# Optimization experiments

Hardware: AMD Instinct MI355X
Metric: run time of the kernel (lower is better)

Reference implementation:

```python
import jax, jax.numpy as jnp
import numpy as np

N = 100000   # nodes
E = 1600000  # edges
F = 64       # input_features == output_features
BN_EPS = 1e-5


def _bn(x, gamma, beta):
    # torch BatchNorm1d (training mode): biased batch statistics
    mu = jnp.mean(x, axis=0)
    var = jnp.var(x, axis=0)
    return (x - mu) * jax.lax.rsqrt(var + BN_EPS) * gamma + beta


def setup_inputs() -> dict:
    key = jax.random.key(0)
    ks = jax.random.split(key, 16)
    s = 0.05
    inp = {
        'node_feats': jax.random.normal(ks[0], (N, F), jnp.float32),
        'edge_feats': jax.random.normal(ks[1], (E, F), jnp.float32),
        'src': jax.random.randint(ks[2], (E,), 0, N, jnp.int32),
        'dst': jax.random.randint(ks[3], (E,), 0, N, jnp.int32),
        # linear params: W [F_in, F_out], b [F_out]
        'W_src_gate': jax.random.normal(ks[4], (F, F), jnp.float32) * s,
        'b_src_gate': jnp.zeros((F,), jnp.float32),
        'W_dst_gate': jax.random.normal(ks[5], (F, F), jnp.float32) * s,
        'b_dst_gate': jnp.zeros((F,), jnp.float32),
        'W_edge_gate': jax.random.normal(ks[6], (F, F), jnp.float32) * s,
        'b_edge_gate': jnp.zeros((F,), jnp.float32),
        'W_src_update': jax.random.normal(ks[7], (F, F), jnp.float32) * s,
        'b_src_update': jnp.zeros((F,), jnp.float32),
        'W_dst_update': jax.random.normal(ks[8], (F, F), jnp.float32) * s,
        'b_dst_update': jnp.zeros((F,), jnp.float32),
        'bn_nodes_gamma': jnp.ones((F,), jnp.float32),
        'bn_nodes_beta': jnp.zeros((F,), jnp.float32),
        'bn_edges_gamma': jnp.ones((F,), jnp.float32),
        'bn_edges_beta': jnp.zeros((F,), jnp.float32),
    }
    return inp


def reference(node_feats, edge_feats, src, dst,
              W_src_gate, b_src_gate, W_dst_gate, b_dst_gate,
              W_edge_gate, b_edge_gate, W_src_update, b_src_update,
              W_dst_update, b_dst_update,
              bn_nodes_gamma, bn_nodes_beta, bn_edges_gamma, bn_edges_beta):
    # EdgeGatedGraphConv (arXiv:1711.07553), residual=True
    e_src = node_feats @ W_src_gate + b_src_gate          # [N,F]
    e_dst = node_feats @ W_dst_gate + b_dst_gate          # [N,F]
    # u_add_v gather + edge transform -> gate logits m [E,F]
    m = e_src[src] + e_dst[dst] + (edge_feats @ W_edge_gate + b_edge_gate)
    sigma = jax.nn.sigmoid(m)                             # [E,F]
    Bh = node_feats @ W_dst_update + b_dst_update         # [N,F]
    # u_mul_e message + scatter-sum to destination nodes
    sum_sigma_h = jax.ops.segment_sum(Bh[src] * sigma, dst, num_segments=node_feats.shape[0])
    sum_sigma = jax.ops.segment_sum(sigma, dst, num_segments=node_feats.shape[0])
    h = sum_sigma_h / (sum_sigma + 1e-6)                  # normalized aggregation
    x = node_feats @ W_src_update + b_src_update + h
    x = jax.nn.silu(_bn(x, bn_nodes_gamma, bn_nodes_beta))
    y = jax.nn.silu(_bn(m, bn_edges_gamma, bn_edges_beta))
    x = node_feats + x   # residual
    y = edge_feats + y   # residual
    return (x, y)
```

## Files before the change

kernel.cpp:

```cpp
#include <hip/hip_runtime.h>
#include <hip/hip_bf16.h>

typedef __attribute__((ext_vector_type(8))) __bf16 bf16x8;
typedef __attribute__((ext_vector_type(4))) float f32x4;

#define MFMA(a,b,c) __builtin_amdgcn_mfma_f32_16x16x32_bf16((a),(b),(c),0,0,0)

__device__ __forceinline__ bf16x8 cvt8(float4 a, float4 b){
  bf16x8 r;
  r[0]=(__bf16)a.x; r[1]=(__bf16)a.y; r[2]=(__bf16)a.z; r[3]=(__bf16)a.w;
  r[4]=(__bf16)b.x; r[5]=(__bf16)b.y; r[6]=(__bf16)b.z; r[7]=(__bf16)b.w;
  return r;
}

__global__ void setup_k(const float* __restrict__ W_sg, const float* __restrict__ W_dg,
                        const float* __restrict__ W_eg, const float* __restrict__ W_su,
                        const float* __restrict__ W_du,
                        bf16x8* __restrict__ Wq,
                        int4* __restrict__ zp, int nz4){
  if (blockIdx.x < 16){
    int tid = blockIdx.x*256 + threadIdx.x;
    if (tid >= 2560) return;
    int lane = tid & 63, g = lane>>4, c = lane&15;
    int frag = (tid>>6)&7, m = tid>>9;
    const float* Ws[5] = {W_eg, W_sg, W_dg, W_du, W_su};
    const float* W = Ws[m];
    int mt = frag>>1, kh = frag&1;
    bf16x8 v;
    #pragma unroll
    for (int j=0;j<8;j++) v[j] = (__bf16)W[(kh*32+g*8+j)*64 + mt*16 + c];
    Wq[tid] = v;
  } else {
    int i = (blockIdx.x-16)*256 + threadIdx.x, st = (gridDim.x-16)*256;
    for (; i<nz4; i+=st) zp[i] = make_int4(0,0,0,0);
  }
}

__global__ __launch_bounds__(256) void xform_hist_k(
    const float* __restrict__ nf, const bf16x8* __restrict__ Wq,
    __bf16* __restrict__ es16, __bf16* __restrict__ ed16,
    __bf16* __restrict__ bh16, float* __restrict__ A_src, int ntiles, int nxf,
    const int* __restrict__ dst, int* __restrict__ cnt, int E)
{
  if ((int)blockIdx.x < nxf){
    int lane = threadIdx.x & 63;
    int gw = blockIdx.x*4 + (threadIdx.x>>6);
    if (gw >= ntiles) return;
    int g = lane>>4, c = lane&15;
    long base = (long)gw*16;
    const float* rp = nf + (base + c)*64 + g*8;
    float4 a0 = *(const float4*)rp,      a1 = *(const float4*)(rp+4);
    float4 a2 = *(const float4*)(rp+32), a3 = *(const float4*)(rp+36);
    bf16x8 B0 = cvt8(a0,a1), B1 = cvt8(a2,a3);
    __bf16* outs[3] = {es16, ed16, bh16};
    const int mats[3] = {1,2,3};
    #pragma unroll
    for (int i=0;i<3;i++){
      #pragma unroll
      for (int mt=0;mt<4;mt++){
        f32x4 am = {0.f,0.f,0.f,0.f};
        am = MFMA(Wq[(mats[i]*8+mt*2+0)*64+lane], B0, am);
        am = MFMA(Wq[(mats[i]*8+mt*2+1)*64+lane], B1, am);
        union { __bf16 h[4]; uint2 u; } pk;
        #pragma unroll
        for (int e=0;e<4;e++) pk.h[e] = (__bf16)am[e];
        *(uint2*)(outs[i] + (base+c)*64 + mt*16 + 4*g) = pk.u;
      }
    }
    #pragma unroll
    for (int mt=0;mt<4;mt++){
      f32x4 am = {0.f,0.f,0.f,0.f};
      am = MFMA(Wq[(4*8+mt*2+0)*64+lane], B0, am);
      am = MFMA(Wq[(4*8+mt*2+1)*64+lane], B1, am);
      *(float4*)(A_src + (base+c)*64 + mt*16 + 4*g) =
        make_float4(am[0],am[1],am[2],am[3]);
    }
  } else {
    int nb = gridDim.x - nxf;
    int i = (blockIdx.x-nxf)*256 + threadIdx.x, st = nb*256;
    for (; i<E; i+=st) atomicAdd(&cnt[dst[i]], 1);
  }
}

__global__ __launch_bounds__(1024) void scan_k(const int* __restrict__ cnt,
                                               int* __restrict__ row, int Nn){
  __shared__ int part[1024];
  int t = threadIdx.x;
  int C = (Nn + 1023) >> 10;
  int lo = t*C;
  int hi = lo + C; if (hi > Nn) hi = Nn;
  int s = 0;
  for (int i=lo; i<hi; i++) s += cnt[i];
  part[t] = s;
  __syncthreads();
  for (int off=1; off<1024; off<<=1){
    int v = part[t];
    int u = (t>=off) ? part[t-off] : 0;
    __syncthreads();
    part[t] = v + u;
    __syncthreads();
  }
  int excl = (t==0) ? 0 : part[t-1];
  for (int i=lo; i<hi; i++){ row[i] = excl; excl += cnt[i]; }
  if (t==1023) row[Nn] = excl;
}

struct T2 {
  float4 e0,e1,e2,e3;
  bf16x8 bs0,bs1,bd0,bd1;
};

__device__ __forceinline__ T2 ld_t2(const float* __restrict__ ef,
                                    const __bf16* __restrict__ es16,
                                    const __bf16* __restrict__ ed16,
                                    long base, int c, int g, int sc, int dc){
  T2 t;
  const float* rpe = ef + (base+c)*64 + g*8;
  t.e0=*(const float4*)rpe;      t.e1=*(const float4*)(rpe+4);
  t.e2=*(const float4*)(rpe+32); t.e3=*(const float4*)(rpe+36);
  t.bs0 = *(const bf16x8*)(es16 + (long)sc*64 + g*8);
  t.bs1 = *(const bf16x8*)(es16 + (long)sc*64 + 32 + g*8);
  t.bd0 = *(const bf16x8*)(ed16 + (long)dc*64 + g*8);
  t.bd1 = *(const bf16x8*)(ed16 + (long)dc*64 + 32 + g*8);
  return t;
}

#define NFILL 1024
__global__ __launch_bounds__(256) void fillA_k(
    const int* __restrict__ src, const int* __restrict__ dst,
    const int* __restrict__ rowp, int* __restrict__ cnt2,
    int2* __restrict__ pairs, int E,
    const float* __restrict__ ef,
    const __bf16* __restrict__ es16, const __bf16* __restrict__ ed16,
    const float* __restrict__ b_sg, const float* __restrict__ b_dg,
    const float* __restrict__ b_eg,
    const bf16x8* __restrict__ Wq,
    __bf16* __restrict__ m16, int ntiles)
{
  __shared__ bf16x8 wl[8*64];
  __shared__ uint2 mst[4][256];
  if (blockIdx.x < NFILL){
    int i = blockIdx.x*256 + threadIdx.x, st = NFILL*256;
    for (; i<E; i+=st){
      int d = dst[i];
      int pos = rowp[d] + atomicAdd(&cnt2[d], 1);
      pairs[pos] = make_int2(i, src[i]);
    }
    return;
  }
  {
    int t = threadIdx.x;
    #pragma unroll
    for (int i=0;i<2;i++) wl[i*256+t] = Wq[i*256+t];
  }
  __syncthreads();
  int lane = threadIdx.x & 63, g = lane>>4, c = lane&15;
  int wv = threadIdx.x>>6;
  bf16x8 I0, I1;
  #pragma unroll
  for (int j=0;j<8;j++){
    I0[j] = (g*8+j == c)      ? (__bf16)1.0f : (__bf16)0.0f;
    I1[j] = (g*8+j == 16 + c) ? (__bf16)1.0f : (__bf16)0.0f;
  }
  int gw = (blockIdx.x-NFILL)*4 + wv;
  int nw = (gridDim.x-NFILL)*4;
  float bias2[4][4];
  #pragma unroll
  for (int mt=0;mt<4;mt++)
    #pragma unroll
    for (int e=0;e<4;e++){
      int f = mt*16 + 4*g + e;
      bias2[mt][e] = b_sg[f] + b_dg[f] + b_eg[f];
    }
  if (gw >= ntiles) return;
  int sc = src[(long)gw*16 + c], dc = dst[(long)gw*16 + c];
  T2 cur = ld_t2(ef, es16, ed16, (long)gw*16, c, g, sc, dc);
  int t1i = gw + nw;
  int sn = sc, dn = dc;
  if (t1i < ntiles){ sn = src[(long)t1i*16 + c]; dn = dst[(long)t1i*16 + c]; }
  int r_o = lane>>3;
  int u0_o = (lane&7)*2;
  for (int tt=gw; tt<ntiles; tt+=nw){
    int t1 = tt + nw;
    T2 nxt;
    if (t1 < ntiles) nxt = ld_t2(ef, es16, ed16, (long)t1*16, c, g, sn, dn);
    int t2 = t1 + nw;
    if (t2 < ntiles){ sn = src[(long)t2*16 + c]; dn = dst[(long)t2*16 + c]; }
    bf16x8 BE0=cvt8(cur.e0,cur.e1), BE1=cvt8(cur.e2,cur.e3);
    #pragma unroll
    for (int mt=0;mt<4;mt++){
      bf16x8 Is = (mt&1) ? I1 : I0;
      f32x4 am = {0.f,0.f,0.f,0.f};
      am = MFMA(wl[(mt*2+0)*64+lane], BE0, am);
      am = MFMA(wl[(mt*2+1)*64+lane], BE1, am);
      am = MFMA(Is, (mt>>1) ? cur.bs1 : cur.bs0, am);
      am = MFMA(Is, (mt>>1) ? cur.bd1 : cur.bd0, am);
      union { __bf16 h[4]; uint2 u; } pk;
      #pragma unroll
      for (int e=0;e<4;e++) pk.h[e] = (__bf16)(am[e] + bias2[mt][e]);
      int u = mt*4 + g;
      mst[wv][c*16 + (u^c)] = pk.u;
    }
    char* tb = (char*)m16 + (size_t)tt*16*128;
    #pragma unroll
    for (int k=0;k<2;k++){
      int r = k*8 + r_o;
      uint2 a = mst[wv][r*16 + ( u0_o      ^ r)];
      uint2 b = mst[wv][r*16 + ((u0_o + 1) ^ r)];
      *(uint4*)(tb + k*1024 + lane*16) = make_uint4(a.x,a.y,b.x,b.y);
    }
    cur = nxt;
  }
}

__global__ __launch_bounds__(256) void phaseB(
    const __bf16* __restrict__ m16, const int2* __restrict__ pairs,
    const __bf16* __restrict__ bh16, const int* __restrict__ rowp,
    const float* __restrict__ b_du, const float* __restrict__ b_su,
    float* __restrict__ A_src,
    float* __restrict__ est, float* __restrict__ nst, int Nn)
{
  __shared__ float sst[256];
  sst[threadIdx.x] = 0.f;
  __syncthreads();
  int lane = threadIdx.x & 63, w = threadIdx.x>>6;
  float bdu = b_du[lane], bsu = b_su[lane];
  int chunk = (Nn + gridDim.x - 1)/gridDim.x;
  int n0 = blockIdx.x*chunk;
  int n1 = n0 + chunk; if (n1 > Nn) n1 = Nn;
  float e1=0.f, e2=0.f, p1=0.f, p2=0.f;
  for (int n=n0+w; n<n1; n+=4){
    int r0 = rowp[n], r1 = rowp[n+1];
    float ssum=0.f, bsum=0.f;
    int r = r0;
    for (; r+8 <= r1; r+=8){
      int2 q[8];
      #pragma unroll
      for (int j=0;j<8;j++) q[j] = pairs[r+j];
      float mv[8], bh[8];
      #pragma unroll
      for (int j=0;j<8;j++) mv[j] = (float)m16[(long)q[j].x*64 + lane];
      #pragma unroll
      for (int j=0;j<8;j++) bh[j] = (float)bh16[(long)q[j].y*64 + lane] + bdu;
      #pragma unroll
      for (int j=0;j<8;j++){
        float sg = 1.f/(1.f+__expf(-mv[j]));
        ssum += sg; bsum += bh[j]*sg;
        e1 += mv[j]; e2 += mv[j]*mv[j];
      }
    }
    for (; r < r1; ++r){
      int2 q0 = pairs[r];
      float mv0 = (float)m16[(long)q0.x*64 + lane];
      float bh0 = (float)bh16[(long)q0.y*64 + lane] + bdu;
      float sg0 = 1.f/(1.f+__expf(-mv0));
      ssum += sg0; bsum += bh0*sg0;
      e1 += mv0;   e2 += mv0*mv0;
    }
    long xi = (long)n*64 + lane;
    float xp = A_src[xi] + bsu + bsum/(ssum+1e-6f);
    A_src[xi] = xp;
    p1 += xp; p2 += xp*xp;
  }
  atomicAdd(&sst[lane],     e1);
  atomicAdd(&sst[64+lane],  e2);
  atomicAdd(&sst[128+lane], p1);
  atomicAdd(&sst[192+lane], p2);
  __syncthreads();
  int t = threadIdx.x;
  if (t < 128) atomicAdd(&est[t], sst[t]);
  else         atomicAdd(&nst[t-128], sst[t]);
}

#define NNF 1024
__global__ __launch_bounds__(256) void finals_k(
    const float* __restrict__ nf, const float* __restrict__ xpre,
    const float* __restrict__ nst, const float* __restrict__ gn,
    const float* __restrict__ btn, float* __restrict__ xo, int Nn,
    const __bf16* __restrict__ m16, const float* __restrict__ ef,
    const float* __restrict__ est, const float* __restrict__ ge,
    const float* __restrict__ bte, float* __restrict__ y, float invE, long E)
{
  if (blockIdx.x < NNF){
    long tid = (long)blockIdx.x*256 + threadIdx.x;
    long stride = (long)NNF*256;
    int col = (int)(tid & 63);
    float invN = 1.f/(float)Nn;
    float mu = nst[col]*invN;
    float var = nst[64+col]*invN - mu*mu;
    float rs = rsqrtf(var + 1e-5f);
    float aa = gn[col]*rs;
    float bb = btn[col] - mu*aa;
    long total = (long)Nn*64;
    for (long i=tid; i<total; i+=stride){
      float z = xpre[i]*aa + bb;
      xo[i] = nf[i] + z/(1.f+__expf(-z));
    }
  } else {
    int oct = threadIdx.x & 7;
    float aa[8], bb[8];
    #pragma unroll
    for (int j=0;j<8;j++){
      int col = oct*8 + j;
      float mu = est[col]*invE;
      float var = est[64+col]*invE - mu*mu;
      float rs = rsqrtf(var + 1e-5f);
      float ga = ge[col]*rs;
      aa[j] = ga; bb[j] = bte[col] - mu*ga;
    }
    long tid = (long)(blockIdx.x-NNF)*256 + threadIdx.x;
    long pstep = ((long)(gridDim.x-NNF)*256) >> 3;
    for (long p = tid>>3; p < E; p += pstep){
      bf16x8 mv = *(const bf16x8*)&m16[p*64 + oct*8];
      const float* rp = ef + p*64 + oct*8;
      float4 f0 = *(const float4*)rp, f1 = *(const float4*)(rp+4);
      float o[8];
      #pragma unroll
      for (int j=0;j<8;j++){
        float z = aa[j]*(float)mv[j] + bb[j];
        float ev = (j<4) ? ((const float*)&f0)[j] : ((const float*)&f1)[j-4];
        o[j] = ev + z/(1.f+__expf(-z));
      }
      float* yp = y + p*64 + oct*8;
      *(float4*)yp     = make_float4(o[0],o[1],o[2],o[3]);
      *(float4*)(yp+4) = make_float4(o[4],o[5],o[6],o[7]);
    }
  }
}

extern "C" void kernel_launch(void* const* d_in, const int* in_sizes, int n_in,
                              void* d_out, int out_size, void* d_ws, size_t ws_size,
                              hipStream_t stream){
  const float* nf  = (const float*)d_in[0];
  const float* ef  = (const float*)d_in[1];
  const int*   src = (const int*)d_in[2];
  const int*   dst = (const int*)d_in[3];
  const float* W_sg=(const float*)d_in[4];  const float* b_sg=(const float*)d_in[5];
  const float* W_dg=(const float*)d_in[6];  const float* b_dg=(const float*)d_in[7];
  const float* W_eg=(const float*)d_in[8];  const float* b_eg=(const float*)d_in[9];
  const float* W_su=(const float*)d_in[10]; const float* b_su=(const float*)d_in[11];
  const float* W_du=(const float*)d_in[12]; const float* b_du=(const float*)d_in[13];
  const float* gn=(const float*)d_in[14];   const float* btn=(const float*)d_in[15];
  const float* ge=(const float*)d_in[16];   const float* bte=(const float*)d_in[17];

  int Nn = in_sizes[0]/64;
  int Ee = in_sizes[2];
  size_t Nf = (size_t)Nn*64;
  size_t Es = (size_t)Ee;

  float* ws    = (float*)d_ws;
  float* A_src = ws;
  __bf16* es16 = (__bf16*)(ws + Nf);
  __bf16* ed16 = (__bf16*)(ws + Nf + Nf/2);
  __bf16* bh16 = (__bf16*)(ws + 2*Nf);
  __bf16* m16  = (__bf16*)(ws + 2*Nf + Nf/2);
  int2*  pairs = (int2*)(ws + 2*Nf + Nf/2 + 32*Es);
  int*   cnt   = (int*)(pairs + Es);
  int*   cnt2  = cnt + Nn;
  float* est   = (float*)(cnt2 + Nn);
  float* nst   = est + 128;
  int*   rowp  = (int*)(nst + 128);
  size_t woff  = 2*Nf + Nf/2 + 32*Es + 2*Es + 2*(size_t)Nn + 256 + (size_t)Nn + 1;
  woff = (woff + 15) & ~(size_t)15;
  bf16x8* Wq   = (bf16x8*)(ws + woff);

  float* xo = (float*)d_out;
  float* yo = xo + Nf;

  int nz4 = (int)((2*(size_t)Nn + 256) >> 2);
  setup_k<<<272,256,0,stream>>>(W_sg,W_dg,W_eg,W_su,W_du,Wq,(int4*)cnt,nz4);

  int ntn = Nn/16;
  int nxf = (ntn+3)/4;
  xform_hist_k<<<nxf+2048,256,0,stream>>>(nf,Wq,es16,ed16,bh16,A_src,ntn,nxf,
                                          dst,cnt,Ee);
  scan_k<<<1,1024,0,stream>>>(cnt,rowp,Nn);
  int nte = Ee/16;
  fillA_k<<<NFILL+4096,256,0,stream>>>(src,dst,rowp,cnt2,pairs,Ee,
                                       ef,es16,ed16,b_sg,b_dg,b_eg,Wq,m16,nte);
  phaseB<<<4096,256,0,stream>>>(m16,pairs,bh16,rowp,b_du,b_su,A_src,est,nst,Nn);
  finals_k<<<NNF+4096,256,0,stream>>>(nf,A_src,nst,gn,btn,xo,Nn,
                                      m16,ef,est,ge,bte,yo,
                                      1.f/(float)Ee,(long)Ee);
}
```

Before: 864.2 us.

## Compute edge BN stats in fill kernel and overlap edge output with aggregation

Edge BatchNorm statistics are now accumulated in the MFMA edge-transform kernel (from fp32 values before bf16 rounding) and reduced via shuffles, shared-memory and global atomics. This removes the e1/e2 work from the gather phase and makes the statistics available one kernel earlier. The edge output pass (y) is then interleaved with the node aggregation in a single kernel using even/odd block assignment, and the node finalization moves into its own small kernel. The aim is to overlap the bandwidth-heavy edge output with the latency-bound gather, at the cost of an extra launch and register pressure in the fill kernel.

```diff
diff --git a/kernel.cpp b/kernel.cpp
--- a/kernel.cpp
+++ b/kernel.cpp
@@ -135,10 +135,11 @@
     const float* __restrict__ b_sg, const float* __restrict__ b_dg,
     const float* __restrict__ b_eg,
     const bf16x8* __restrict__ Wq,
-    __bf16* __restrict__ m16, int ntiles)
+    __bf16* __restrict__ m16, float* __restrict__ est, int ntiles)
 {
   __shared__ bf16x8 wl[8*64];
   __shared__ uint2 mst[4][256];
+  __shared__ float sst2[128];
   if (blockIdx.x < NFILL){
     int i = blockIdx.x*256 + threadIdx.x, st = NFILL*256;
     for (; i<E; i+=st){
@@ -152,6 +153,7 @@
     int t = threadIdx.x;
     #pragma unroll
     for (int i=0;i<2;i++) wl[i*256+t] = Wq[i*256+t];
+    if (t < 128) sst2[t] = 0.f;
   }
   __syncthreads();
   int lane = threadIdx.x & 63, g = lane>>4, c = lane&15;
@@ -164,138 +166,134 @@
   }
   int gw = (blockIdx.x-NFILL)*4 + wv;
   int nw = (gridDim.x-NFILL)*4;
-  float bias2[4][4];
+  float bias2[4][4], es1[4][4], es2[4][4];
   #pragma unroll
   for (int mt=0;mt<4;mt++)
     #pragma unroll
     for (int e=0;e<4;e++){
       int f = mt*16 + 4*g + e;
       bias2[mt][e] = b_sg[f] + b_dg[f] + b_eg[f];
-    }
-  if (gw >= ntiles) return;
-  int sc = src[(long)gw*16 + c], dc = dst[(long)gw*16 + c];
-  T2 cur = ld_t2(ef, es16, ed16, (long)gw*16, c, g, sc, dc);
-  int t1i = gw + nw;
-  int sn = sc, dn = dc;
-  if (t1i < ntiles){ sn = src[(long)t1i*16 + c]; dn = dst[(long)t1i*16 + c]; }
-  int r_o = lane>>3;
-  int u0_o = (lane&7)*2;
-  for (int tt=gw; tt<ntiles; tt+=nw){
-    int t1 = tt + nw;
-    T2 nxt;
-    if (t1 < ntiles) nxt = ld_t2(ef, es16, ed16, (long)t1*16, c, g, sn, dn);
-    int t2 = t1 + nw;
-    if (t2 < ntiles){ sn = src[(long)t2*16 + c]; dn = dst[(long)t2*16 + c]; }
-    bf16x8 BE0=cvt8(cur.e0,cur.e1), BE1=cvt8(cur.e2,cur.e3);
-    #pragma unroll
-    for (int mt=0;mt<4;mt++){
-      bf16x8 Is = (mt&1) ? I1 : I0;
-      f32x4 am = {0.f,0.f,0.f,0.f};
-      am = MFMA(wl[(mt*2+0)*64+lane], BE0, am);
-      am = MFMA(wl[(mt*2+1)*64+lane], BE1, am);
-      am = MFMA(Is, (mt>>1) ? cur.bs1 : cur.bs0, am);
-      am = MFMA(Is, (mt>>1) ? cur.bd1 : cur.bd0, am);
-      union { __bf16 h[4]; uint2 u; } pk;
+      es1[mt][e] = 0.f; es2[mt][e] = 0.f;
+    }
+  if (gw < ntiles){
+    int sc = src[(long)gw*16 + c], dc = dst[(long)gw*16 + c];
+    T2 cur = ld_t2(ef, es16, ed16, (long)gw*16, c, g, sc, dc);
+    int t1i = gw + nw;
+    int sn = sc, dn = dc;
+    if (t1i < ntiles){ sn = src[(long)t1i*16 + c]; dn = dst[(long)t1i*16 + c]; }
+    int r_o = lane>>3;
+    int u0_o = (lane&7)*2;
+    for (int tt=gw; tt<ntiles; tt+=nw){
+      int t1 = tt + nw;
+      T2 nxt;
+      if (t1 < ntiles) nxt = ld_t2(ef, es16, ed16, (long)t1*16, c, g, sn, dn);
+      int t2 = t1 + nw;
+      if (t2 < ntiles){ sn = src[(long)t2*16 + c]; dn = dst[(long)t2*16 + c]; }
+      bf16x8 BE0=cvt8(cur.e0,cur.e1), BE1=cvt8(cur.e2,cur.e3);
       #pragma unroll
-      for (int e=0;e<4;e++) pk.h[e] = (__bf16)(am[e] + bias2[mt][e]);
-      int u = mt*4 + g;
-      mst[wv][c*16 + (u^c)] = pk.u;
-    }
-    char* tb = (char*)m16 + (size_t)tt*16*128;
-    #pragma unroll
-    for (int k=0;k<2;k++){
-      int r = k*8 + r_o;
-      uint2 a = mst[wv][r*16 + ( u0_o      ^ r)];
-      uint2 b = mst[wv][r*16 + ((u0_o + 1) ^ r)];
-      *(uint4*)(tb + k*1024 + lane*16) = make_uint4(a.x,a.y,b.x,b.y);
-    }
-    cur = nxt;
-  }
-}
-
-__global__ __launch_bounds__(256) void phaseB(
+      for (int mt=0;mt<4;mt++){
+        bf16x8 Is = (mt&1) ? I1 : I0;
+        f32x4 am = {0.f,0.f,0.f,0.f};
+        am = MFMA(wl[(mt*2+0)*64+lane], BE0, am);
+        am = MFMA(wl[(mt*2+1)*64+lane], BE1, am);
+        am = MFMA(Is, (mt>>1) ? cur.bs1 : cur.bs0, am);
+        am = MFMA(Is, (mt>>1) ? cur.bd1 : cur.bd0, am);
+        union { __bf16 h[4]; uint2 u; } pk;
+        #pragma unroll
+        for (int e=0;e<4;e++){
+          float mv = am[e] + bias2[mt][e];
+          es1[mt][e] += mv; es2[mt][e] += mv*mv;
+          pk.h[e] = (__bf16)mv;
+        }
+        int u = mt*4 + g;
+        mst[wv][c*16 + (u^c)] = pk.u;
+      }
+      char* tb = (char*)m16 + (size_t)tt*16*128;
+      #pragma unroll
+      for (int k=0;k<2;k++){
+        int r = k*8 + r_o;
+        uint2 a = mst[wv][r*16 + ( u0_o      ^ r)];
+        uint2 b = mst[wv][r*16 + ((u0_o + 1) ^ r)];
+        *(uint4*)(tb + k*1024 + lane*16) = make_uint4(a.x,a.y,b.x,b.y);
+      }
+      cur = nxt;
+    }
+  }
+  #pragma unroll
+  for (int mt=0;mt<4;mt++)
+    #pragma unroll
+    for (int e=0;e<4;e++){
+      float a = es1[mt][e], b = es2[mt][e];
+      a += __shfl_xor(a,1,64); a += __shfl_xor(a,2,64);
+      a += __shfl_xor(a,4,64); a += __shfl_xor(a,8,64);
+      b += __shfl_xor(b,1,64); b += __shfl_xor(b,2,64);
+      b += __shfl_xor(b,4,64); b += __shfl_xor(b,8,64);
+      if (c == 0){
+        int f = mt*16 + 4*g + e;
+        atomicAdd(&sst2[f],    a);
+        atomicAdd(&sst2[64+f], b);
+      }
+    }
+  __syncthreads();
+  if (threadIdx.x < 128) atomicAdd(&est[threadIdx.x], sst2[threadIdx.x]);
+}
+
+__global__ __launch_bounds__(256) void bz_k(
     const __bf16* __restrict__ m16, const int2* __restrict__ pairs,
     const __bf16* __restrict__ bh16, const int* __restrict__ rowp,
     const float* __restrict__ b_du, const float* __restrict__ b_su,
-    float* __restrict__ A_src,
-    float* __restrict__ est, float* __restrict__ nst, int Nn)
+    float* __restrict__ A_src, float* __restrict__ nst, int Nn,
+    const float* __restrict__ ef, const float* __restrict__ est,
+    const float* __restrict__ ge, const float* __restrict__ bte,
+    float* __restrict__ y, float invE, long E)
 {
-  __shared__ float sst[256];
-  sst[threadIdx.x] = 0.f;
-  __syncthreads();
-  int lane = threadIdx.x & 63, w = threadIdx.x>>6;
-  float bdu = b_du[lane], bsu = b_su[lane];
-  int chunk = (Nn + gridDim.x - 1)/gridDim.x;
-  int n0 = blockIdx.x*chunk;
-  int n1 = n0 + chunk; if (n1 > Nn) n1 = Nn;
-  float e1=0.f, e2=0.f, p1=0.f, p2=0.f;
-  for (int n=n0+w; n<n1; n+=4){
-    int r0 = rowp[n], r1 = rowp[n+1];
-    float ssum=0.f, bsum=0.f;
-    int r = r0;
-    for (; r+8 <= r1; r+=8){
-      int2 q[8];
-      #pragma unroll
-      for (int j=0;j<8;j++) q[j] = pairs[r+j];
-      float mv[8], bh[8];
-      #pragma unroll
-      for (int j=0;j<8;j++) mv[j] = (float)m16[(long)q[j].x*64 + lane];
-      #pragma unroll
-      for (int j=0;j<8;j++) bh[j] = (float)bh16[(long)q[j].y*64 + lane] + bdu;
-      #pragma unroll
-      for (int j=0;j<8;j++){
-        float sg = 1.f/(1.f+__expf(-mv[j]));
-        ssum += sg; bsum += bh[j]*sg;
-        e1 += mv[j]; e2 += mv[j]*mv[j];
-      }
-    }
-    for (; r < r1; ++r){
-      int2 q0 = pairs[r];
-      float mv0 = (float)m16[(long)q0.x*64 + lane];
-      float bh0 = (float)bh16[(long)q0.y*64 + lane] + bdu;
-      float sg0 = 1.f/(1.f+__expf(-mv0));
-      ssum += sg0; bsum += bh0*sg0;
-      e1 += mv0;   e2 += mv0*mv0;
-    }
-    long xi = (long)n*64 + lane;
-    float xp = A_src[xi] + bsu + bsum/(ssum+1e-6f);
-    A_src[xi] = xp;
-    p1 += xp; p2 += xp*xp;
-  }
-  atomicAdd(&sst[lane],     e1);
-  atomicAdd(&sst[64+lane],  e2);
-  atomicAdd(&sst[128+lane], p1);
-  atomicAdd(&sst[192+lane], p2);
-  __syncthreads();
-  int t = threadIdx.x;
-  if (t < 128) atomicAdd(&est[t], sst[t]);
-  else         atomicAdd(&nst[t-128], sst[t]);
-}
-
-#define NNF 1024
-__global__ __launch_bounds__(256) void finals_k(
-    const float* __restrict__ nf, const float* __restrict__ xpre,
-    const float* __restrict__ nst, const float* __restrict__ gn,
-    const float* __restrict__ btn, float* __restrict__ xo, int Nn,
-    const __bf16* __restrict__ m16, const float* __restrict__ ef,
-    const float* __restrict__ est, const float* __restrict__ ge,
-    const float* __restrict__ bte, float* __restrict__ y, float invE, long E)
-{
-  if (blockIdx.x < NNF){
-    long tid = (long)blockIdx.x*256 + threadIdx.x;
-    long stride = (long)NNF*256;
-    int col = (int)(tid & 63);
-    float invN = 1.f/(float)Nn;
-    float mu = nst[col]*invN;
-    float var = nst[64+col]*invN - mu*mu;
-    float rs = rsqrtf(var + 1e-5f);
-    float aa = gn[col]*rs;
-    float bb = btn[col] - mu*aa;
-    long total = (long)Nn*64;
-    for (long i=tid; i<total; i+=stride){
-      float z = xpre[i]*aa + bb;
-      xo[i] = nf[i] + z/(1.f+__expf(-z));
-    }
+  int half = gridDim.x >> 1;
+  if ((blockIdx.x & 1) == 0){
+    __shared__ float sst[128];
+    if (threadIdx.x < 128) sst[threadIdx.x] = 0.f;
+    __syncthreads();
+    int vb = blockIdx.x >> 1;
+    int lane = threadIdx.x & 63, w = threadIdx.x>>6;
+    float bdu = b_du[lane], bsu = b_su[lane];
+    int chunk = (Nn + half - 1)/half;
+    int n0 = vb*chunk;
+    int n1 = n0 + chunk; if (n1 > Nn) n1 = Nn;
+    float p1=0.f, p2=0.f;
+    for (int n=n0+w; n<n1; n+=4){
+      int r0 = rowp[n], r1 = rowp[n+1];
+      float ssum=0.f, bsum=0.f;
+      int r = r0;
+      for (; r+8 <= r1; r+=8){
+        int2 q[8];
+        #pragma unroll
+        for (int j=0;j<8;j++) q[j] = pairs[r+j];
+        float mv[8], bh[8];
+        #pragma unroll
+        for (int j=0;j<8;j++) mv[j] = (float)m16[(long)q[j].x*64 + lane];
+        #pragma unroll
+        for (int j=0;j<8;j++) bh[j] = (float)bh16[(long)q[j].y*64 + lane] + bdu;
+        #pragma unroll
+        for (int j=0;j<8;j++){
+          float sg = 1.f/(1.f+__expf(-mv[j]));
+          ssum += sg; bsum += bh[j]*sg;
+        }
+      }
+      for (; r < r1; ++r){
+        int2 q0 = pairs[r];
+        float mv0 = (float)m16[(long)q0.x*64 + lane];
+        float bh0 = (float)bh16[(long)q0.y*64 + lane] + bdu;
+        float sg0 = 1.f/(1.f+__expf(-mv0));
+        ssum += sg0; bsum += bh0*sg0;
+      }
+      long xi = (long)n*64 + lane;
+      float xp = A_src[xi] + bsu + bsum/(ssum+1e-6f);
+      A_src[xi] = xp;
+      p1 += xp; p2 += xp*xp;
+    }
+    atomicAdd(&sst[lane],    p1);
+    atomicAdd(&sst[64+lane], p2);
+    __syncthreads();
+    if (threadIdx.x < 128) atomicAdd(&nst[threadIdx.x], sst[threadIdx.x]);
   } else {
     int oct = threadIdx.x & 7;
     float aa[8], bb[8];
@@ -308,8 +306,9 @@
       float ga = ge[col]*rs;
       aa[j] = ga; bb[j] = bte[col] - mu*ga;
     }
-    long tid = (long)(blockIdx.x-NNF)*256 + threadIdx.x;
-    long pstep = ((long)(gridDim.x-NNF)*256) >> 3;
+    int vy = blockIdx.x >> 1;
+    long tid = (long)vy*256 + threadIdx.x;
+    long pstep = ((long)half*256) >> 3;
     for (long p = tid>>3; p < E; p += pstep){
       bf16x8 mv = *(const bf16x8*)&m16[p*64 + oct*8];
       const float* rp = ef + p*64 + oct*8;
@@ -325,6 +324,27 @@
       *(float4*)yp     = make_float4(o[0],o[1],o[2],o[3]);
       *(float4*)(yp+4) = make_float4(o[4],o[5],o[6],o[7]);
     }
+  }
+}
+
+__global__ __launch_bounds__(256) void xfin_k(
+    const float* __restrict__ nf, const float* __restrict__ xpre,
+    const float* __restrict__ nst, const float* __restrict__ gn,
+    const float* __restrict__ btn, float* __restrict__ xo, int Nn)
+{
+  long tid = (long)blockIdx.x*256 + threadIdx.x;
+  long stride = (long)gridDim.x*256;
+  int col = (int)(tid & 63);
+  float invN = 1.f/(float)Nn;
+  float mu = nst[col]*invN;
+  float var = nst[64+col]*invN - mu*mu;
+  float rs = rsqrtf(var + 1e-5f);
+  float aa = gn[col]*rs;
+  float bb = btn[col] - mu*aa;
+  long total = (long)Nn*64;
+  for (long i=tid; i<total; i+=stride){
+    float z = xpre[i]*aa + bb;
+    xo[i] = nf[i] + z/(1.f+__expf(-z));
   }
 }
 
@@ -377,9 +397,8 @@
   scan_k<<<1,1024,0,stream>>>(cnt,rowp,Nn);
   int nte = Ee/16;
   fillA_k<<<NFILL+4096,256,0,stream>>>(src,dst,rowp,cnt2,pairs,Ee,
-                                       ef,es16,ed16,b_sg,b_dg,b_eg,Wq,m16,nte);
-  phaseB<<<4096,256,0,stream>>>(m16,pairs,bh16,rowp,b_du,b_su,A_src,est,nst,Nn);
-  finals_k<<<NNF+4096,256,0,stream>>>(nf,A_src,nst,gn,btn,xo,Nn,
-                                      m16,ef,est,ge,bte,yo,
-                                      1.f/(float)Ee,(long)Ee);
-}
+                                       ef,es16,ed16,b_sg,b_dg,b_eg,Wq,m16,est,nte);
+  bz_k<<<4096,256,0,stream>>>(m16,pairs,bh16,rowp,b_du,b_su,A_src,nst,Nn,
+                              ef,est,ge,bte,yo,1.f/(float)Ee,(long)Ee);
+  xfin_k<<<1024,256,0,stream>>>(nf,A_src,nst,gn,btn,xo,Nn);
+}
```

After: 865.1 us. Within noise of the previous version (+0.1%).
